# Kernel optimization log

Hardware: AMD Instinct MI355X
Metric: run time of the kernel (lower is better)

## Reference

```python
import jax, jax.numpy as jnp
import numpy as np

B, N, T, L = 4, 512, 288, 128
NEG_SLOPE = 0.2
TEMPERATURE = 0.2
CLAMP = 10.0
EPS = 1e-10


def setup_inputs() -> dict:
    key = jax.random.key(0)
    ks = jax.random.split(key, 6)
    s_in = 1.0 / np.sqrt(T)
    s_lat = 1.0 / np.sqrt(2 * L)
    s_b = 1.0 / np.sqrt(L)
    x = jax.random.normal(ks[0], (B, N, T), dtype=jnp.float32)
    W1 = jax.random.normal(ks[1], (L, T), dtype=jnp.float32) * s_in
    W2 = jax.random.normal(ks[2], (L, T), dtype=jnp.float32) * s_in
    Wp = jax.random.normal(ks[3], (L, 2 * L), dtype=jnp.float32) * s_lat
    Wb = jax.random.normal(ks[4], (L,), dtype=jnp.float32) * s_b
    noise = jnp.clip(jax.random.uniform(ks[5], (N, N), dtype=jnp.float32), 1e-6, 1.0 - 1e-6)
    return {
        "x": x,
        "W1": W1, "b1": jnp.zeros((L,), jnp.float32),
        "W2": W2, "b2": jnp.zeros((L,), jnp.float32),
        "Wp": Wp, "bp": jnp.zeros((L,), jnp.float32),
        "Wb": Wb, "bb": jnp.zeros((1,), jnp.float32),
        "noise": noise,
    }


def _leaky(v):
    return jnp.where(v >= 0, v, NEG_SLOPE * v)


def reference(x, W1, b1, W2, b2, Wp, bp, Wb, bb, noise):
    # per-node projections (B, N, L)
    x1 = _leaky(jnp.einsum('bnt,lt->bnl', x, W1) + b1)
    x2 = _leaky(jnp.einsum('bnt,lt->bnl', x, W2) + b2)
    # linear_para_latent(cat(x1_i, x2_j)) == x1_i @ Wp_a^T + x2_j @ Wp_b^T + bp
    Wp_a, Wp_b = Wp[:, :L], Wp[:, L:]
    s1 = jnp.einsum('bnl,ml->bnm', x1, Wp_a)  # (B, N, L_out)
    s2 = jnp.einsum('bnl,ml->bnm', x2, Wp_b)
    pair = s1[:, :, None, :] + s2[:, None, :, :] + bp  # (B, N, N, L)
    h = _leaky(pair)
    logits = jnp.einsum('bijl,l->bij', h, Wb) + bb[0]  # (B, N, N)
    p = jax.nn.sigmoid(logits).mean(axis=0)            # (N, N)
    p = p * (1.0 - jnp.eye(N, dtype=p.dtype))          # fill_diagonal_(0)
    # relaxed Bernoulli sample (binary concrete) with logit clamping
    logit_p = jnp.clip(jnp.log(p + EPS) - jnp.log1p(-p + EPS), -CLAMP, CLAMP)
    logistic = jnp.log(noise) - jnp.log1p(-noise)
    adj = jax.nn.sigmoid((logit_p + logistic) / TEMPERATURE)
    return adj
```

## Files before the change

kernel.cpp:

```cpp
#include <hip/hip_runtime.h>
#include <hip/hip_bf16.h>
#include <math.h>

#define NB 4
#define NN 512
#define NT 288
#define NL 128

__global__ __launch_bounds__(512) void kA(
    const float* __restrict__ x,
    const float* __restrict__ W1,
    const float* __restrict__ b1,
    const float* __restrict__ W2,
    const float* __restrict__ b2,
    const float* __restrict__ Wp,
    const float* __restrict__ bp,
    const float* __restrict__ Wb,
    const float* __restrict__ bb,
    float* __restrict__ S12,
    float* __restrict__ Aarr,
    float* __restrict__ Carr)
{
    __shared__ __align__(16) float xs[8 * NT];
    __shared__ __align__(16) float x12s[8 * 256];
    __shared__ __align__(16) float ph[8 * 256];

    const int t = threadIdx.x;
    const int bn0 = blockIdx.x * 8;
    const int col = t & 255;
    const int kh = t >> 8;

    for (int q = 0; q < 2; ++q) {
        int idx = q * 512 + t;
        if (idx < 576) {
            int row = idx / 72, c4 = idx % 72;
            *(float4*)&xs[row * NT + c4 * 4] =
                *(const float4*)&x[(size_t)(bn0 + row) * NT + c4 * 4];
        }
    }
    __syncthreads();

    const float* wrow = ((col < 128) ? (W1 + col * NT) : (W2 + (col - 128) * NT))
                        + kh * 144;
    const float bias1 = (col < 128) ? b1[col] : b2[col - 128];
    const int kb1 = kh * 144;

    float acc[8];
#pragma unroll
    for (int n = 0; n < 8; ++n) acc[n] = 0.0f;

    for (int k = 0; k < 144; k += 4) {
        float4 w = *(const float4*)(wrow + k);
#pragma unroll
        for (int n = 0; n < 8; ++n) {
            float4 xv = *(const float4*)&xs[n * NT + kb1 + k];
            acc[n] = fmaf(w.x, xv.x, acc[n]);
            acc[n] = fmaf(w.y, xv.y, acc[n]);
            acc[n] = fmaf(w.z, xv.z, acc[n]);
            acc[n] = fmaf(w.w, xv.w, acc[n]);
        }
    }
    if (kh) {
#pragma unroll
        for (int n = 0; n < 8; ++n) ph[n * 256 + col] = acc[n];
    }
    __syncthreads();
    if (!kh) {
#pragma unroll
        for (int n = 0; n < 8; ++n) {
            float v = acc[n] + ph[n * 256 + col] + bias1;
            x12s[n * 256 + col] = fmaxf(v, 0.2f * v);
        }
    }
    __syncthreads();

    const int koff = (col < 128) ? 0 : 128;
    const float* wprow = ((col < 128) ? (Wp + col * 256) : (Wp + (col - 128) * 256 + 128))
                         + kh * 64;
    const float bias2 = (col < 128) ? bp[col] : 0.0f;
    const int kb2 = koff + kh * 64;

    float acc2[8];
#pragma unroll
    for (int n = 0; n < 8; ++n) acc2[n] = 0.0f;

    for (int k = 0; k < 64; k += 4) {
        float4 w = *(const float4*)(wprow + k);
#pragma unroll
        for (int n = 0; n < 8; ++n) {
            float4 xv = *(const float4*)&x12s[n * 256 + kb2 + k];
            acc2[n] = fmaf(w.x, xv.x, acc2[n]);
            acc2[n] = fmaf(w.y, xv.y, acc2[n]);
            acc2[n] = fmaf(w.z, xv.z, acc2[n]);
            acc2[n] = fmaf(w.w, xv.w, acc2[n]);
        }
    }
    if (kh) {
#pragma unroll
        for (int n = 0; n < 8; ++n) ph[n * 256 + col] = acc2[n];
    }
    __syncthreads();

    float* s12s = xs;
    if (!kh) {
#pragma unroll
        for (int n = 0; n < 8; ++n) {
            float sv = acc2[n] + ph[n * 256 + col] + bias2;
            S12[(size_t)(bn0 + n) * 256 + col] = sv;
            s12s[n * 257 + col] = sv;
        }
    }
    __syncthreads();

    {
        int lane32 = t & 31;
        int n = (t >> 5) & 7;
        int isC = t >> 8;
        int base = isC ? 128 : 0;
        float sum = 0.0f;
#pragma unroll
        for (int s = 0; s < 4; ++s) {
            int j = lane32 + s * 32;
            sum = fmaf(s12s[n * 257 + base + j], Wb[j], sum);
        }
#pragma unroll
        for (int m = 16; m >= 1; m >>= 1)
            sum += __shfl_xor(sum, m, 32);
        if (lane32 == 0) {
            if (isC) Carr[bn0 + n] = 0.6f * sum;
            else     Aarr[bn0 + n] = 0.6f * sum + bb[0];
        }
    }
}

__global__ __launch_bounds__(512) void kB(
    const float* __restrict__ S12,
    const float* __restrict__ Aarr,
    const float* __restrict__ Carr,
    const float* __restrict__ Wb,
    float* __restrict__ PS4)
{
    __shared__ __align__(16) float S1t[128 * 64];
    __shared__ __align__(16) float S2t[128 * 64];
    __shared__ __align__(16) float wbs[128];

    const int t = threadIdx.x;
    const int bx = blockIdx.x, by = blockIdx.y, bz = blockIdx.z;
    const int ibn0 = bz * NN + bx * 64;
    const int jbn0 = bz * NN + by * 64;

    if (t < 32) *(float4*)&wbs[t * 4] = *(const float4*)&Wb[t * 4];

#pragma unroll
    for (int q = 0; q < 4; ++q) {
        int idx = q * 512 + t;
        int row = idx >> 5;
        int c4 = idx & 31;
        float4 v1 = *(const float4*)&S12[(size_t)(ibn0 + row) * 256 + c4 * 4];
        float4 v2 = *(const float4*)&S12[(size_t)(jbn0 + row) * 256 + 128 + c4 * 4];
        float a1[4] = {v1.x, v1.y, v1.z, v1.w};
        float a2[4] = {v2.x, v2.y, v2.z, v2.w};
#pragma unroll
        for (int d = 0; d < 4; ++d) {
            int l = c4 * 4 + d;
            int sw = ((l >> 2) & 15) << 2;
            S1t[l * 64 + (row ^ sw)] = a1[d];
            S2t[l * 64 + (row ^ sw)] = a2[d];
        }
    }
    __syncthreads();

    const int tid = t & 255;
    const int lh = t >> 8;
    const int tx = tid & 15, ty = tid >> 4;
    const int i0 = ty * 4, j0 = tx * 4;
    const int lbase = lh * 64;

    float accv[16];
#pragma unroll
    for (int k = 0; k < 16; ++k) accv[k] = 0.0f;

    for (int l4 = 0; l4 < 16; ++l4) {
        const int sw = l4 << 2;
        const int lrow = (lbase + l4 * 4) * 64;
        float4 wv = *(const float4*)&wbs[lbase + l4 * 4];
        const float wl[4] = {wv.x, wv.y, wv.z, wv.w};
#pragma unroll
        for (int d = 0; d < 4; ++d) {
            float4 a = *(const float4*)&S1t[lrow + d * 64 + (i0 ^ sw)];
            float4 b = *(const float4*)&S2t[lrow + d * 64 + (j0 ^ sw)];
            float w = wl[d];
            float ai[4] = {a.x, a.y, a.z, a.w};
            float bj[4] = {b.x, b.y, b.z, b.w};
#pragma unroll
            for (int ii = 0; ii < 4; ++ii)
#pragma unroll
                for (int jj = 0; jj < 4; ++jj) {
                    float tv = ai[ii] + bj[jj];
                    accv[ii * 4 + jj] = fmaf(fabsf(tv), w, accv[ii * 4 + jj]);
                }
        }
    }

    float* red = S1t;
    __syncthreads();
    if (lh) {
#pragma unroll
        for (int q = 0; q < 4; ++q) {
            float4 v = {accv[4 * q], accv[4 * q + 1], accv[4 * q + 2], accv[4 * q + 3]};
            *(float4*)&red[q * 1024 + tid * 4] = v;
        }
    }
    __syncthreads();
    if (!lh) {
#pragma unroll
        for (int q = 0; q < 4; ++q) {
            float4 v = *(const float4*)&red[q * 1024 + tid * 4];
            accv[4 * q]     += v.x;
            accv[4 * q + 1] += v.y;
            accv[4 * q + 2] += v.z;
            accv[4 * q + 3] += v.w;
        }

        float Av[4], Cv[4];
#pragma unroll
        for (int ii = 0; ii < 4; ++ii) Av[ii] = Aarr[ibn0 + i0 + ii];
#pragma unroll
        for (int jj = 0; jj < 4; ++jj) Cv[jj] = Carr[jbn0 + j0 + jj];

#pragma unroll
        for (int ii = 0; ii < 4; ++ii) {
            float4 o;
            float* op = (float*)&o;
#pragma unroll
            for (int jj = 0; jj < 4; ++jj) {
                float lg = Av[ii] + Cv[jj] + 0.4f * accv[ii * 4 + jj];
                op[jj] = 1.0f / (1.0f + expf(-lg));
            }
            *(float4*)&PS4[(size_t)bz * (NN * NN) +
                           (size_t)(bx * 64 + i0 + ii) * NN + by * 64 + j0] = o;
        }
    }
}

__global__ __launch_bounds__(256) void kF(
    const float* __restrict__ PS4,
    const float* __restrict__ noise,
    float* __restrict__ out)
{
    int g = blockIdx.x * 256 + threadIdx.x;
    int f = g * 2;
    int i = f >> 9;
    int jbase = f & 511;

    float2 s0 = *(const float2*)&PS4[f];
    float2 s1 = *(const float2*)&PS4[262144 + f];
    float2 s2 = *(const float2*)&PS4[524288 + f];
    float2 s3 = *(const float2*)&PS4[786432 + f];
    float2 nz = *(const float2*)&noise[f];

    float ps[2] = {s0.x + s1.x + s2.x + s3.x,
                   s0.y + s1.y + s2.y + s3.y};
    float nv[2] = {nz.x, nz.y};

    float2 o;
    float* op = (float*)&o;
#pragma unroll
    for (int c = 0; c < 2; ++c) {
        float p = 0.25f * ps[c];
        if (jbase + c == i) p = 0.0f;
        float lp = logf(p + 1e-10f) - log1pf(-p + 1e-10f);
        lp = fminf(fmaxf(lp, -10.0f), 10.0f);
        float lgs = logf(nv[c]) - log1pf(-nv[c]);
        op[c] = 1.0f / (1.0f + expf(-(lp + lgs) * 5.0f));
    }
    *(float2*)&out[f] = o;
}

extern "C" void kernel_launch(void* const* d_in, const int* in_sizes, int n_in,
                              void* d_out, int out_size, void* d_ws, size_t ws_size,
                              hipStream_t stream) {
    const float* x     = (const float*)d_in[0];
    const float* W1    = (const float*)d_in[1];
    const float* b1    = (const float*)d_in[2];
    const float* W2    = (const float*)d_in[3];
    const float* b2    = (const float*)d_in[4];
    const float* Wp    = (const float*)d_in[5];
    const float* bp    = (const float*)d_in[6];
    const float* Wb    = (const float*)d_in[7];
    const float* bb    = (const float*)d_in[8];
    const float* noise = (const float*)d_in[9];

    float* ws   = (float*)d_ws;
    float* S12  = ws;
    float* Aarr = ws + 524288;
    float* Carr = Aarr + 2048;
    float* PS4  = Carr + 2048;

    kA<<<256, 512, 0, stream>>>(x, W1, b1, W2, b2, Wp, bp, Wb, bb, S12, Aarr, Carr);
    kB<<<dim3(8, 8, 4), 512, 0, stream>>>(S12, Aarr, Carr, Wb, PS4);
    kF<<<512, 256, 0, stream>>>(PS4, noise, (float*)d_out);
}
```

Measured before the change: 44.82 us.

## Fuse three kernels into one cooperative kernel with grid-wide syncs

Merges the projection, pairwise logit and final sampling kernels into a single cooperative launch of 256 blocks, replacing the kernel boundaries with grid.sync barriers. The aim is to remove the launch overhead and inter-kernel gaps of the two extra launches. In exchange, the cooperative launch and grid barriers add their own cost, shared memory grows to the union of the stages' footprints, and all 256 blocks must be co-resident.

```diff
diff --git a/kernel.cpp b/kernel.cpp
--- a/kernel.cpp
+++ b/kernel.cpp
@@ -1,13 +1,16 @@
 #include <hip/hip_runtime.h>
 #include <hip/hip_bf16.h>
+#include <hip/hip_cooperative_groups.h>
 #include <math.h>
+
+namespace cg = cooperative_groups;
 
 #define NB 4
 #define NN 512
 #define NT 288
 #define NL 128
 
-__global__ __launch_bounds__(512) void kA(
+__global__ __launch_bounds__(512) void mega(
     const float* __restrict__ x,
     const float* __restrict__ W1,
     const float* __restrict__ b1,
@@ -17,264 +20,267 @@
     const float* __restrict__ bp,
     const float* __restrict__ Wb,
     const float* __restrict__ bb,
+    const float* __restrict__ noise,
     float* __restrict__ S12,
     float* __restrict__ Aarr,
-    float* __restrict__ Carr)
-{
-    __shared__ __align__(16) float xs[8 * NT];
-    __shared__ __align__(16) float x12s[8 * 256];
-    __shared__ __align__(16) float ph[8 * 256];
-
-    const int t = threadIdx.x;
-    const int bn0 = blockIdx.x * 8;
-    const int col = t & 255;
-    const int kh = t >> 8;
-
-    for (int q = 0; q < 2; ++q) {
-        int idx = q * 512 + t;
-        if (idx < 576) {
-            int row = idx / 72, c4 = idx % 72;
-            *(float4*)&xs[row * NT + c4 * 4] =
-                *(const float4*)&x[(size_t)(bn0 + row) * NT + c4 * 4];
-        }
-    }
-    __syncthreads();
-
-    const float* wrow = ((col < 128) ? (W1 + col * NT) : (W2 + (col - 128) * NT))
-                        + kh * 144;
-    const float bias1 = (col < 128) ? b1[col] : b2[col - 128];
-    const int kb1 = kh * 144;
-
-    float acc[8];
-#pragma unroll
-    for (int n = 0; n < 8; ++n) acc[n] = 0.0f;
-
-    for (int k = 0; k < 144; k += 4) {
-        float4 w = *(const float4*)(wrow + k);
-#pragma unroll
-        for (int n = 0; n < 8; ++n) {
-            float4 xv = *(const float4*)&xs[n * NT + kb1 + k];
-            acc[n] = fmaf(w.x, xv.x, acc[n]);
-            acc[n] = fmaf(w.y, xv.y, acc[n]);
-            acc[n] = fmaf(w.z, xv.z, acc[n]);
-            acc[n] = fmaf(w.w, xv.w, acc[n]);
-        }
-    }
-    if (kh) {
-#pragma unroll
-        for (int n = 0; n < 8; ++n) ph[n * 256 + col] = acc[n];
-    }
-    __syncthreads();
-    if (!kh) {
-#pragma unroll
-        for (int n = 0; n < 8; ++n) {
-            float v = acc[n] + ph[n * 256 + col] + bias1;
-            x12s[n * 256 + col] = fmaxf(v, 0.2f * v);
-        }
-    }
-    __syncthreads();
-
-    const int koff = (col < 128) ? 0 : 128;
-    const float* wprow = ((col < 128) ? (Wp + col * 256) : (Wp + (col - 128) * 256 + 128))
-                         + kh * 64;
-    const float bias2 = (col < 128) ? bp[col] : 0.0f;
-    const int kb2 = koff + kh * 64;
-
-    float acc2[8];
-#pragma unroll
-    for (int n = 0; n < 8; ++n) acc2[n] = 0.0f;
-
-    for (int k = 0; k < 64; k += 4) {
-        float4 w = *(const float4*)(wprow + k);
-#pragma unroll
-        for (int n = 0; n < 8; ++n) {
-            float4 xv = *(const float4*)&x12s[n * 256 + kb2 + k];
-            acc2[n] = fmaf(w.x, xv.x, acc2[n]);
-            acc2[n] = fmaf(w.y, xv.y, acc2[n]);
-            acc2[n] = fmaf(w.z, xv.z, acc2[n]);
-            acc2[n] = fmaf(w.w, xv.w, acc2[n]);
-        }
-    }
-    if (kh) {
-#pragma unroll
-        for (int n = 0; n < 8; ++n) ph[n * 256 + col] = acc2[n];
-    }
-    __syncthreads();
-
-    float* s12s = xs;
-    if (!kh) {
-#pragma unroll
-        for (int n = 0; n < 8; ++n) {
-            float sv = acc2[n] + ph[n * 256 + col] + bias2;
-            S12[(size_t)(bn0 + n) * 256 + col] = sv;
-            s12s[n * 257 + col] = sv;
-        }
-    }
-    __syncthreads();
-
-    {
-        int lane32 = t & 31;
-        int n = (t >> 5) & 7;
-        int isC = t >> 8;
-        int base = isC ? 128 : 0;
-        float sum = 0.0f;
-#pragma unroll
-        for (int s = 0; s < 4; ++s) {
-            int j = lane32 + s * 32;
-            sum = fmaf(s12s[n * 257 + base + j], Wb[j], sum);
-        }
-#pragma unroll
-        for (int m = 16; m >= 1; m >>= 1)
-            sum += __shfl_xor(sum, m, 32);
-        if (lane32 == 0) {
-            if (isC) Carr[bn0 + n] = 0.6f * sum;
-            else     Aarr[bn0 + n] = 0.6f * sum + bb[0];
-        }
-    }
-}
-
-__global__ __launch_bounds__(512) void kB(
-    const float* __restrict__ S12,
-    const float* __restrict__ Aarr,
-    const float* __restrict__ Carr,
-    const float* __restrict__ Wb,
-    float* __restrict__ PS4)
-{
-    __shared__ __align__(16) float S1t[128 * 64];
-    __shared__ __align__(16) float S2t[128 * 64];
-    __shared__ __align__(16) float wbs[128];
-
-    const int t = threadIdx.x;
-    const int bx = blockIdx.x, by = blockIdx.y, bz = blockIdx.z;
-    const int ibn0 = bz * NN + bx * 64;
-    const int jbn0 = bz * NN + by * 64;
-
-    if (t < 32) *(float4*)&wbs[t * 4] = *(const float4*)&Wb[t * 4];
-
-#pragma unroll
-    for (int q = 0; q < 4; ++q) {
-        int idx = q * 512 + t;
-        int row = idx >> 5;
-        int c4 = idx & 31;
-        float4 v1 = *(const float4*)&S12[(size_t)(ibn0 + row) * 256 + c4 * 4];
-        float4 v2 = *(const float4*)&S12[(size_t)(jbn0 + row) * 256 + 128 + c4 * 4];
-        float a1[4] = {v1.x, v1.y, v1.z, v1.w};
-        float a2[4] = {v2.x, v2.y, v2.z, v2.w};
-#pragma unroll
-        for (int d = 0; d < 4; ++d) {
-            int l = c4 * 4 + d;
-            int sw = ((l >> 2) & 15) << 2;
-            S1t[l * 64 + (row ^ sw)] = a1[d];
-            S2t[l * 64 + (row ^ sw)] = a2[d];
-        }
-    }
-    __syncthreads();
-
-    const int tid = t & 255;
-    const int lh = t >> 8;
-    const int tx = tid & 15, ty = tid >> 4;
-    const int i0 = ty * 4, j0 = tx * 4;
-    const int lbase = lh * 64;
-
-    float accv[16];
-#pragma unroll
-    for (int k = 0; k < 16; ++k) accv[k] = 0.0f;
-
-    for (int l4 = 0; l4 < 16; ++l4) {
-        const int sw = l4 << 2;
-        const int lrow = (lbase + l4 * 4) * 64;
-        float4 wv = *(const float4*)&wbs[lbase + l4 * 4];
-        const float wl[4] = {wv.x, wv.y, wv.z, wv.w};
-#pragma unroll
-        for (int d = 0; d < 4; ++d) {
-            float4 a = *(const float4*)&S1t[lrow + d * 64 + (i0 ^ sw)];
-            float4 b = *(const float4*)&S2t[lrow + d * 64 + (j0 ^ sw)];
-            float w = wl[d];
-            float ai[4] = {a.x, a.y, a.z, a.w};
-            float bj[4] = {b.x, b.y, b.z, b.w};
-#pragma unroll
-            for (int ii = 0; ii < 4; ++ii)
-#pragma unroll
-                for (int jj = 0; jj < 4; ++jj) {
-                    float tv = ai[ii] + bj[jj];
-                    accv[ii * 4 + jj] = fmaf(fabsf(tv), w, accv[ii * 4 + jj]);
-                }
-        }
-    }
-
-    float* red = S1t;
-    __syncthreads();
-    if (lh) {
-#pragma unroll
-        for (int q = 0; q < 4; ++q) {
-            float4 v = {accv[4 * q], accv[4 * q + 1], accv[4 * q + 2], accv[4 * q + 3]};
-            *(float4*)&red[q * 1024 + tid * 4] = v;
-        }
-    }
-    __syncthreads();
-    if (!lh) {
-#pragma unroll
-        for (int q = 0; q < 4; ++q) {
-            float4 v = *(const float4*)&red[q * 1024 + tid * 4];
-            accv[4 * q]     += v.x;
-            accv[4 * q + 1] += v.y;
-            accv[4 * q + 2] += v.z;
-            accv[4 * q + 3] += v.w;
-        }
-
-        float Av[4], Cv[4];
-#pragma unroll
-        for (int ii = 0; ii < 4; ++ii) Av[ii] = Aarr[ibn0 + i0 + ii];
-#pragma unroll
-        for (int jj = 0; jj < 4; ++jj) Cv[jj] = Carr[jbn0 + j0 + jj];
-
-#pragma unroll
-        for (int ii = 0; ii < 4; ++ii) {
-            float4 o;
-            float* op = (float*)&o;
-#pragma unroll
-            for (int jj = 0; jj < 4; ++jj) {
-                float lg = Av[ii] + Cv[jj] + 0.4f * accv[ii * 4 + jj];
-                op[jj] = 1.0f / (1.0f + expf(-lg));
-            }
-            *(float4*)&PS4[(size_t)bz * (NN * NN) +
-                           (size_t)(bx * 64 + i0 + ii) * NN + by * 64 + j0] = o;
-        }
-    }
-}
-
-__global__ __launch_bounds__(256) void kF(
-    const float* __restrict__ PS4,
-    const float* __restrict__ noise,
+    float* __restrict__ Carr,
+    float* __restrict__ PS4,
     float* __restrict__ out)
 {
-    int g = blockIdx.x * 256 + threadIdx.x;
-    int f = g * 2;
-    int i = f >> 9;
-    int jbase = f & 511;
-
-    float2 s0 = *(const float2*)&PS4[f];
-    float2 s1 = *(const float2*)&PS4[262144 + f];
-    float2 s2 = *(const float2*)&PS4[524288 + f];
-    float2 s3 = *(const float2*)&PS4[786432 + f];
-    float2 nz = *(const float2*)&noise[f];
-
-    float ps[2] = {s0.x + s1.x + s2.x + s3.x,
-                   s0.y + s1.y + s2.y + s3.y};
-    float nv[2] = {nz.x, nz.y};
-
-    float2 o;
-    float* op = (float*)&o;
-#pragma unroll
-    for (int c = 0; c < 2; ++c) {
-        float p = 0.25f * ps[c];
-        if (jbase + c == i) p = 0.0f;
-        float lp = logf(p + 1e-10f) - log1pf(-p + 1e-10f);
-        lp = fminf(fmaxf(lp, -10.0f), 10.0f);
-        float lgs = logf(nv[c]) - log1pf(-nv[c]);
-        op[c] = 1.0f / (1.0f + expf(-(lp + lgs) * 5.0f));
+    __shared__ __align__(16) float smem[16512];
+    cg::grid_group grid = cg::this_grid();
+
+    const int t = threadIdx.x;
+
+    {
+        float* xs   = smem;
+        float* x12s = smem + 2304;
+        float* ph   = smem + 4352;
+
+        const int bn0 = blockIdx.x * 8;
+        const int col = t & 255;
+        const int kh = t >> 8;
+
+        for (int q = 0; q < 2; ++q) {
+            int idx = q * 512 + t;
+            if (idx < 576) {
+                int row = idx / 72, c4 = idx % 72;
+                *(float4*)&xs[row * NT + c4 * 4] =
+                    *(const float4*)&x[(size_t)(bn0 + row) * NT + c4 * 4];
+            }
+        }
+        __syncthreads();
+
+        const float* wrow = ((col < 128) ? (W1 + col * NT) : (W2 + (col - 128) * NT))
+                            + kh * 144;
+        const float bias1 = (col < 128) ? b1[col] : b2[col - 128];
+        const int kb1 = kh * 144;
+
+        float acc[8];
+#pragma unroll
+        for (int n = 0; n < 8; ++n) acc[n] = 0.0f;
+
+        for (int k = 0; k < 144; k += 4) {
+            float4 w = *(const float4*)(wrow + k);
+#pragma unroll
+            for (int n = 0; n < 8; ++n) {
+                float4 xv = *(const float4*)&xs[n * NT + kb1 + k];
+                acc[n] = fmaf(w.x, xv.x, acc[n]);
+                acc[n] = fmaf(w.y, xv.y, acc[n]);
+                acc[n] = fmaf(w.z, xv.z, acc[n]);
+                acc[n] = fmaf(w.w, xv.w, acc[n]);
+            }
+        }
+        if (kh) {
+#pragma unroll
+            for (int n = 0; n < 8; ++n) ph[n * 256 + col] = acc[n];
+        }
+        __syncthreads();
+        if (!kh) {
+#pragma unroll
+            for (int n = 0; n < 8; ++n) {
+                float v = acc[n] + ph[n * 256 + col] + bias1;
+                x12s[n * 256 + col] = fmaxf(v, 0.2f * v);
+            }
+        }
+        __syncthreads();
+
+        const int koff = (col < 128) ? 0 : 128;
+        const float* wprow = ((col < 128) ? (Wp + col * 256) : (Wp + (col - 128) * 256 + 128))
+                             + kh * 64;
+        const float bias2 = (col < 128) ? bp[col] : 0.0f;
+        const int kb2 = koff + kh * 64;
+
+        float acc2[8];
+#pragma unroll
+        for (int n = 0; n < 8; ++n) acc2[n] = 0.0f;
+
+        for (int k = 0; k < 64; k += 4) {
+            float4 w = *(const float4*)(wprow + k);
+#pragma unroll
+            for (int n = 0; n < 8; ++n) {
+                float4 xv = *(const float4*)&x12s[n * 256 + kb2 + k];
+                acc2[n] = fmaf(w.x, xv.x, acc2[n]);
+                acc2[n] = fmaf(w.y, xv.y, acc2[n]);
+                acc2[n] = fmaf(w.z, xv.z, acc2[n]);
+                acc2[n] = fmaf(w.w, xv.w, acc2[n]);
+            }
+        }
+        if (kh) {
+#pragma unroll
+            for (int n = 0; n < 8; ++n) ph[n * 256 + col] = acc2[n];
+        }
+        __syncthreads();
+
+        float* s12s = xs;
+        if (!kh) {
+#pragma unroll
+            for (int n = 0; n < 8; ++n) {
+                float sv = acc2[n] + ph[n * 256 + col] + bias2;
+                S12[(size_t)(bn0 + n) * 256 + col] = sv;
+                s12s[n * 257 + col] = sv;
+            }
+        }
+        __syncthreads();
+
+        {
+            int lane32 = t & 31;
+            int n = (t >> 5) & 7;
+            int isC = t >> 8;
+            int base = isC ? 128 : 0;
+            float sum = 0.0f;
+#pragma unroll
+            for (int s = 0; s < 4; ++s) {
+                int j = lane32 + s * 32;
+                sum = fmaf(s12s[n * 257 + base + j], Wb[j], sum);
+            }
+#pragma unroll
+            for (int m = 16; m >= 1; m >>= 1)
+                sum += __shfl_xor(sum, m, 32);
+            if (lane32 == 0) {
+                if (isC) Carr[bn0 + n] = 0.6f * sum;
+                else     Aarr[bn0 + n] = 0.6f * sum + bb[0];
+            }
+        }
     }
-    *(float2*)&out[f] = o;
+
+    grid.sync();
+
+    {
+        float* S1t = smem;
+        float* S2t = smem + 8192;
+        float* wbs = smem + 16384;
+
+        const int bx = blockIdx.x & 7;
+        const int by = (blockIdx.x >> 3) & 7;
+        const int bz = blockIdx.x >> 6;
+        const int ibn0 = bz * NN + bx * 64;
+        const int jbn0 = bz * NN + by * 64;
+
+        if (t < 32) *(float4*)&wbs[t * 4] = *(const float4*)&Wb[t * 4];
+
+#pragma unroll
+        for (int q = 0; q < 4; ++q) {
+            int idx = q * 512 + t;
+            int row = idx >> 5;
+            int c4 = idx & 31;
+            float4 v1 = *(const float4*)&S12[(size_t)(ibn0 + row) * 256 + c4 * 4];
+            float4 v2 = *(const float4*)&S12[(size_t)(jbn0 + row) * 256 + 128 + c4 * 4];
+            float a1[4] = {v1.x, v1.y, v1.z, v1.w};
+            float a2[4] = {v2.x, v2.y, v2.z, v2.w};
+#pragma unroll
+            for (int d = 0; d < 4; ++d) {
+                int l = c4 * 4 + d;
+                int sw = ((l >> 2) & 15) << 2;
+                S1t[l * 64 + (row ^ sw)] = a1[d];
+                S2t[l * 64 + (row ^ sw)] = a2[d];
+            }
+        }
+        __syncthreads();
+
+        const int tid = t & 255;
+        const int lh = t >> 8;
+        const int tx = tid & 15, ty = tid >> 4;
+        const int i0 = ty * 4, j0 = tx * 4;
+        const int lbase = lh * 64;
+
+        float accv[16];
+#pragma unroll
+        for (int k = 0; k < 16; ++k) accv[k] = 0.0f;
+
+        for (int l4 = 0; l4 < 16; ++l4) {
+            const int sw = l4 << 2;
+            const int lrow = (lbase + l4 * 4) * 64;
+            float4 wv = *(const float4*)&wbs[lbase + l4 * 4];
+            const float wl[4] = {wv.x, wv.y, wv.z, wv.w};
+#pragma unroll
+            for (int d = 0; d < 4; ++d) {
+                float4 a = *(const float4*)&S1t[lrow + d * 64 + (i0 ^ sw)];
+                float4 b = *(const float4*)&S2t[lrow + d * 64 + (j0 ^ sw)];
+                float w = wl[d];
+                float ai[4] = {a.x, a.y, a.z, a.w};
+                float bj[4] = {b.x, b.y, b.z, b.w};
+#pragma unroll
+                for (int ii = 0; ii < 4; ++ii)
+#pragma unroll
+                    for (int jj = 0; jj < 4; ++jj) {
+                        float tv = ai[ii] + bj[jj];
+                        accv[ii * 4 + jj] = fmaf(fabsf(tv), w, accv[ii * 4 + jj]);
+                    }
+            }
+        }
+
+        float* red = S1t;
+        __syncthreads();
+        if (lh) {
+#pragma unroll
+            for (int q = 0; q < 4; ++q) {
+                float4 v = {accv[4 * q], accv[4 * q + 1], accv[4 * q + 2], accv[4 * q + 3]};
+                *(float4*)&red[q * 1024 + tid * 4] = v;
+            }
+        }
+        __syncthreads();
+        if (!lh) {
+#pragma unroll
+            for (int q = 0; q < 4; ++q) {
+                float4 v = *(const float4*)&red[q * 1024 + tid * 4];
+                accv[4 * q]     += v.x;
+                accv[4 * q + 1] += v.y;
+                accv[4 * q + 2] += v.z;
+                accv[4 * q + 3] += v.w;
+            }
+
+            float Av[4], Cv[4];
+#pragma unroll
+            for (int ii = 0; ii < 4; ++ii) Av[ii] = Aarr[ibn0 + i0 + ii];
+#pragma unroll
+            for (int jj = 0; jj < 4; ++jj) Cv[jj] = Carr[jbn0 + j0 + jj];
+
+#pragma unroll
+            for (int ii = 0; ii < 4; ++ii) {
+                float4 o;
+                float* op = (float*)&o;
+#pragma unroll
+                for (int jj = 0; jj < 4; ++jj) {
+                    float lg = Av[ii] + Cv[jj] + 0.4f * accv[ii * 4 + jj];
+                    op[jj] = 1.0f / (1.0f + expf(-lg));
+                }
+                *(float4*)&PS4[(size_t)bz * (NN * NN) +
+                               (size_t)(bx * 64 + i0 + ii) * NN + by * 64 + j0] = o;
+            }
+        }
+    }
+
+    grid.sync();
+
+    {
+        int f = blockIdx.x * 1024 + t * 2;
+        int i = f >> 9;
+        int jbase = f & 511;
+
+        float2 s0 = *(const float2*)&PS4[f];
+        float2 s1 = *(const float2*)&PS4[262144 + f];
+        float2 s2 = *(const float2*)&PS4[524288 + f];
+        float2 s3 = *(const float2*)&PS4[786432 + f];
+        float2 nz = *(const float2*)&noise[f];
+
+        float ps[2] = {s0.x + s1.x + s2.x + s3.x,
+                       s0.y + s1.y + s2.y + s3.y};
+        float nv[2] = {nz.x, nz.y};
+
+        float2 o;
+        float* op = (float*)&o;
+#pragma unroll
+        for (int c = 0; c < 2; ++c) {
+            float p = 0.25f * ps[c];
+            if (jbase + c == i) p = 0.0f;
+            float lp = logf(p + 1e-10f) - log1pf(-p + 1e-10f);
+            lp = fminf(fmaxf(lp, -10.0f), 10.0f);
+            float lgs = logf(nv[c]) - log1pf(-nv[c]);
+            op[c] = 1.0f / (1.0f + expf(-(lp + lgs) * 5.0f));
+        }
+        *(float2*)&out[f] = o;
+    }
 }
 
 extern "C" void kernel_launch(void* const* d_in, const int* in_sizes, int n_in,
@@ -296,8 +302,13 @@
     float* Aarr = ws + 524288;
     float* Carr = Aarr + 2048;
     float* PS4  = Carr + 2048;
-
-    kA<<<256, 512, 0, stream>>>(x, W1, b1, W2, b2, Wp, bp, Wb, bb, S12, Aarr, Carr);
-    kB<<<dim3(8, 8, 4), 512, 0, stream>>>(S12, Aarr, Carr, Wb, PS4);
-    kF<<<512, 256, 0, stream>>>(PS4, noise, (float*)d_out);
+    float* out  = (float*)d_out;
+
+    void* params[] = {
+        (void*)&x, (void*)&W1, (void*)&b1, (void*)&W2, (void*)&b2,
+        (void*)&Wp, (void*)&bp, (void*)&Wb, (void*)&bb, (void*)&noise,
+        (void*)&S12, (void*)&Aarr, (void*)&Carr, (void*)&PS4, (void*)&out
+    };
+    hipLaunchCooperativeKernel((const void*)mega, dim3(256), dim3(512),
+                               params, 0, stream);
 }
```

Result: slower. 105.7 us (+135.8%).

## Fuse finalize into pair kernel via atomics and last-block counter; stage weights in LDS

Applied to the files above, without the earlier changes.

The batch-sum and binary-concrete finalize kernel is removed. The pair kernel now atomically accumulates sigmoids into a shared P buffer, and the last of the four batch blocks per tile, found with a counter, applies the noise/logit transform. The projection kernel zeroes P and the counters, stages weight tiles transposed into swizzled LDS, and reads x directly from global memory instead of LDS. This saves a launch and the PS4 round trip, at the cost of float atomics with nondeterministic summation order and extra barrier-heavy weight staging.

```diff
diff --git a/kernel.cpp b/kernel.cpp
--- a/kernel.cpp
+++ b/kernel.cpp
@@ -2,12 +2,9 @@
 #include <hip/hip_bf16.h>
 #include <math.h>
 
-#define NB 4
 #define NN 512
-#define NT 288
-#define NL 128
-
-__global__ __launch_bounds__(512) void kA(
+
+__global__ __launch_bounds__(512) void kP(
     const float* __restrict__ x,
     const float* __restrict__ W1,
     const float* __restrict__ b1,
@@ -19,47 +16,71 @@
     const float* __restrict__ bb,
     float* __restrict__ S12,
     float* __restrict__ Aarr,
-    float* __restrict__ Carr)
+    float* __restrict__ Carr,
+    float* __restrict__ P,
+    int*   __restrict__ cnt)
 {
-    __shared__ __align__(16) float xs[8 * NT];
+    __shared__ __align__(16) float Wt[2][16][256];
     __shared__ __align__(16) float x12s[8 * 256];
     __shared__ __align__(16) float ph[8 * 256];
-
-    const int t = threadIdx.x;
+    __shared__ __align__(16) float s12s[8 * 257];
+
+    const int t   = threadIdx.x;
     const int bn0 = blockIdx.x * 8;
     const int col = t & 255;
-    const int kh = t >> 8;
-
-    for (int q = 0; q < 2; ++q) {
-        int idx = q * 512 + t;
-        if (idx < 576) {
-            int row = idx / 72, c4 = idx % 72;
-            *(float4*)&xs[row * NT + c4 * 4] =
-                *(const float4*)&x[(size_t)(bn0 + row) * NT + c4 * 4];
-        }
-    }
-    __syncthreads();
-
-    const float* wrow = ((col < 128) ? (W1 + col * NT) : (W2 + (col - 128) * NT))
-                        + kh * 144;
+    const int kh  = t >> 8;
+    const int khu = __builtin_amdgcn_readfirstlane(kh);
+    const int cq  = col >> 2, cj = col & 3;
+
+    *(float2*)&P[(size_t)(blockIdx.x * 512 + t) * 2] = make_float2(0.f, 0.f);
+    if (blockIdx.x == 0 && t < 64) cnt[t] = 0;
+
+    float acc[8];
+#pragma unroll
+    for (int n = 0; n < 8; ++n) acc[n] = 0.0f;
+
+    for (int c = 0; c < 9; ++c) {
+#pragma unroll
+        for (int i = 0; i < 4; ++i) {
+            int task = i * 512 + t;
+            int kk   = task & 15;
+            int cq_s = (task >> 4) & 63;
+            int khs  = task >> 10;
+            int kb   = khs * 144 + c * 16 + kk;
+            float4 v;
+#pragma unroll
+            for (int j = 0; j < 4; ++j) {
+                int r = cq_s * 4 + j;
+                const float* wr = (r < 128) ? (W1 + (size_t)r * 288)
+                                            : (W2 + (size_t)(r - 128) * 288);
+                ((float*)&v)[j] = wr[kb];
+            }
+            *(float4*)&Wt[khs][kk][((cq_s ^ kk) & 63) * 4] = v;
+        }
+        __syncthreads();
+
+        const int kb0 = khu * 144 + c * 16;
+#pragma unroll
+        for (int k4 = 0; k4 < 4; ++k4) {
+            float w[4];
+#pragma unroll
+            for (int d = 0; d < 4; ++d) {
+                int k = k4 * 4 + d;
+                w[d] = Wt[kh][k][((cq ^ k) & 63) * 4 + cj];
+            }
+#pragma unroll
+            for (int n = 0; n < 8; ++n) {
+                float4 xv = *(const float4*)&x[(size_t)(bn0 + n) * 288 + kb0 + k4 * 4];
+                acc[n] = fmaf(w[0], xv.x, acc[n]);
+                acc[n] = fmaf(w[1], xv.y, acc[n]);
+                acc[n] = fmaf(w[2], xv.z, acc[n]);
+                acc[n] = fmaf(w[3], xv.w, acc[n]);
+            }
+        }
+        __syncthreads();
+    }
+
     const float bias1 = (col < 128) ? b1[col] : b2[col - 128];
-    const int kb1 = kh * 144;
-
-    float acc[8];
-#pragma unroll
-    for (int n = 0; n < 8; ++n) acc[n] = 0.0f;
-
-    for (int k = 0; k < 144; k += 4) {
-        float4 w = *(const float4*)(wrow + k);
-#pragma unroll
-        for (int n = 0; n < 8; ++n) {
-            float4 xv = *(const float4*)&xs[n * NT + kb1 + k];
-            acc[n] = fmaf(w.x, xv.x, acc[n]);
-            acc[n] = fmaf(w.y, xv.y, acc[n]);
-            acc[n] = fmaf(w.z, xv.z, acc[n]);
-            acc[n] = fmaf(w.w, xv.w, acc[n]);
-        }
-    }
     if (kh) {
 #pragma unroll
         for (int n = 0; n < 8; ++n) ph[n * 256 + col] = acc[n];
@@ -74,34 +95,58 @@
     }
     __syncthreads();
 
-    const int koff = (col < 128) ? 0 : 128;
-    const float* wprow = ((col < 128) ? (Wp + col * 256) : (Wp + (col - 128) * 256 + 128))
-                         + kh * 64;
+    float acc2[8];
+#pragma unroll
+    for (int n = 0; n < 8; ++n) acc2[n] = 0.0f;
+
+    for (int c = 0; c < 4; ++c) {
+#pragma unroll
+        for (int i = 0; i < 4; ++i) {
+            int task = i * 512 + t;
+            int kk   = task & 15;
+            int cq_s = (task >> 4) & 63;
+            int khs  = task >> 10;
+            int kb   = khs * 64 + c * 16 + kk;
+            float4 v;
+#pragma unroll
+            for (int j = 0; j < 4; ++j) {
+                int r = cq_s * 4 + j;
+                const float* src = (r < 128) ? (Wp + (size_t)r * 256 + kb)
+                                             : (Wp + (size_t)(r - 128) * 256 + 128 + kb);
+                ((float*)&v)[j] = *src;
+            }
+            *(float4*)&Wt[khs][kk][((cq_s ^ kk) & 63) * 4] = v;
+        }
+        __syncthreads();
+
+        const int koff = (col < 128) ? 0 : 128;
+        const int kb0  = koff + kh * 64 + c * 16;
+#pragma unroll
+        for (int k4 = 0; k4 < 4; ++k4) {
+            float w[4];
+#pragma unroll
+            for (int d = 0; d < 4; ++d) {
+                int k = k4 * 4 + d;
+                w[d] = Wt[kh][k][((cq ^ k) & 63) * 4 + cj];
+            }
+#pragma unroll
+            for (int n = 0; n < 8; ++n) {
+                float4 xv = *(const float4*)&x12s[n * 256 + kb0 + k4 * 4];
+                acc2[n] = fmaf(w[0], xv.x, acc2[n]);
+                acc2[n] = fmaf(w[1], xv.y, acc2[n]);
+                acc2[n] = fmaf(w[2], xv.z, acc2[n]);
+                acc2[n] = fmaf(w[3], xv.w, acc2[n]);
+            }
+        }
+        __syncthreads();
+    }
+
     const float bias2 = (col < 128) ? bp[col] : 0.0f;
-    const int kb2 = koff + kh * 64;
-
-    float acc2[8];
-#pragma unroll
-    for (int n = 0; n < 8; ++n) acc2[n] = 0.0f;
-
-    for (int k = 0; k < 64; k += 4) {
-        float4 w = *(const float4*)(wprow + k);
-#pragma unroll
-        for (int n = 0; n < 8; ++n) {
-            float4 xv = *(const float4*)&x12s[n * 256 + kb2 + k];
-            acc2[n] = fmaf(w.x, xv.x, acc2[n]);
-            acc2[n] = fmaf(w.y, xv.y, acc2[n]);
-            acc2[n] = fmaf(w.z, xv.z, acc2[n]);
-            acc2[n] = fmaf(w.w, xv.w, acc2[n]);
-        }
-    }
     if (kh) {
 #pragma unroll
         for (int n = 0; n < 8; ++n) ph[n * 256 + col] = acc2[n];
     }
     __syncthreads();
-
-    float* s12s = xs;
     if (!kh) {
 #pragma unroll
         for (int n = 0; n < 8; ++n) {
@@ -133,16 +178,20 @@
     }
 }
 
-__global__ __launch_bounds__(512) void kB(
+__global__ __launch_bounds__(512) void kQ(
     const float* __restrict__ S12,
     const float* __restrict__ Aarr,
     const float* __restrict__ Carr,
     const float* __restrict__ Wb,
-    float* __restrict__ PS4)
+    const float* __restrict__ noise,
+    float* __restrict__ P,
+    int*   __restrict__ cnt,
+    float* __restrict__ out)
 {
     __shared__ __align__(16) float S1t[128 * 64];
     __shared__ __align__(16) float S2t[128 * 64];
     __shared__ __align__(16) float wbs[128];
+    __shared__ int lastf;
 
     const int t = threadIdx.x;
     const int bx = blockIdx.x, by = blockIdx.y, bz = blockIdx.z;
@@ -229,52 +278,50 @@
         for (int jj = 0; jj < 4; ++jj) Cv[jj] = Carr[jbn0 + j0 + jj];
 
 #pragma unroll
-        for (int ii = 0; ii < 4; ++ii) {
-            float4 o;
-            float* op = (float*)&o;
+        for (int ii = 0; ii < 4; ++ii)
 #pragma unroll
             for (int jj = 0; jj < 4; ++jj) {
                 float lg = Av[ii] + Cv[jj] + 0.4f * accv[ii * 4 + jj];
-                op[jj] = 1.0f / (1.0f + expf(-lg));
-            }
-            *(float4*)&PS4[(size_t)bz * (NN * NN) +
-                           (size_t)(bx * 64 + i0 + ii) * NN + by * 64 + j0] = o;
-        }
-    }
-}
-
-__global__ __launch_bounds__(256) void kF(
-    const float* __restrict__ PS4,
-    const float* __restrict__ noise,
-    float* __restrict__ out)
-{
-    int g = blockIdx.x * 256 + threadIdx.x;
-    int f = g * 2;
-    int i = f >> 9;
-    int jbase = f & 511;
-
-    float2 s0 = *(const float2*)&PS4[f];
-    float2 s1 = *(const float2*)&PS4[262144 + f];
-    float2 s2 = *(const float2*)&PS4[524288 + f];
-    float2 s3 = *(const float2*)&PS4[786432 + f];
-    float2 nz = *(const float2*)&noise[f];
-
-    float ps[2] = {s0.x + s1.x + s2.x + s3.x,
-                   s0.y + s1.y + s2.y + s3.y};
-    float nv[2] = {nz.x, nz.y};
-
-    float2 o;
-    float* op = (float*)&o;
-#pragma unroll
-    for (int c = 0; c < 2; ++c) {
-        float p = 0.25f * ps[c];
-        if (jbase + c == i) p = 0.0f;
-        float lp = logf(p + 1e-10f) - log1pf(-p + 1e-10f);
-        lp = fminf(fmaxf(lp, -10.0f), 10.0f);
-        float lgs = logf(nv[c]) - log1pf(-nv[c]);
-        op[c] = 1.0f / (1.0f + expf(-(lp + lgs) * 5.0f));
-    }
-    *(float2*)&out[f] = o;
+                float sig = 1.0f / (1.0f + expf(-lg));
+                atomicAdd(&P[(size_t)(bx * 64 + i0 + ii) * NN + by * 64 + j0 + jj], sig);
+            }
+    }
+
+    __syncthreads();
+    if (t == 0) {
+        __threadfence();
+        int old = atomicAdd(&cnt[bx * 8 + by], 1);
+        lastf = (old == 3) ? 1 : 0;
+    }
+    __syncthreads();
+    if (lastf) {
+        __threadfence();
+        int r  = t >> 3;
+        int cg = (t & 7) * 8;
+        int gi = bx * 64 + r;
+        size_t base = (size_t)gi * NN + by * 64 + cg;
+
+        float4 p0 = *(const float4*)&P[base];
+        float4 p1 = *(const float4*)&P[base + 4];
+        float4 n0 = *(const float4*)&noise[base];
+        float4 n1 = *(const float4*)&noise[base + 4];
+
+        float pv[8] = {p0.x, p0.y, p0.z, p0.w, p1.x, p1.y, p1.z, p1.w};
+        float nv[8] = {n0.x, n0.y, n0.z, n0.w, n1.x, n1.y, n1.z, n1.w};
+        float ov[8];
+#pragma unroll
+        for (int c = 0; c < 8; ++c) {
+            float p = 0.25f * pv[c];
+            int gj = by * 64 + cg + c;
+            if (gj == gi) p = 0.0f;
+            float lp = logf(p + 1e-10f) - log1pf(-p + 1e-10f);
+            lp = fminf(fmaxf(lp, -10.0f), 10.0f);
+            float lgs = logf(nv[c]) - log1pf(-nv[c]);
+            ov[c] = 1.0f / (1.0f + expf(-(lp + lgs) * 5.0f));
+        }
+        *(float4*)&out[base]     = make_float4(ov[0], ov[1], ov[2], ov[3]);
+        *(float4*)&out[base + 4] = make_float4(ov[4], ov[5], ov[6], ov[7]);
+    }
 }
 
 extern "C" void kernel_launch(void* const* d_in, const int* in_sizes, int n_in,
@@ -295,9 +342,11 @@
     float* S12  = ws;
     float* Aarr = ws + 524288;
     float* Carr = Aarr + 2048;
-    float* PS4  = Carr + 2048;
-
-    kA<<<256, 512, 0, stream>>>(x, W1, b1, W2, b2, Wp, bp, Wb, bb, S12, Aarr, Carr);
-    kB<<<dim3(8, 8, 4), 512, 0, stream>>>(S12, Aarr, Carr, Wb, PS4);
-    kF<<<512, 256, 0, stream>>>(PS4, noise, (float*)d_out);
+    float* P    = Carr + 2048;
+    int*   cnt  = (int*)(P + 262144);
+
+    kP<<<256, 512, 0, stream>>>(x, W1, b1, W2, b2, Wp, bp, Wb, bb,
+                                S12, Aarr, Carr, P, cnt);
+    kQ<<<dim3(8, 8, 4), 512, 0, stream>>>(S12, Aarr, Carr, Wb, noise,
+                                          P, cnt, (float*)d_out);
 }
```

Measured after the change: 80.38 us. 79.3% more time.
